# Optimization experiments

Measured on AMD Instinct MI355X. Metric: run time of the kernel, lower is better.

The kernel has to match this reference:

```python
import jax, jax.numpy as jnp
import numpy as np

B, T, N, CIN = 64, 24, 256, 1  # batch, n_his, n stations, in channels
F1, F2, OUTC = 64, 128, 1      # blocks [[64,64],[64,128]], output channels
K = 3                          # conv kernel size


def conv2d_same(x, w):  # x [B,H,W,C], w [K,K,C,O]
    return jax.lax.conv_general_dilated(x, w, (1, 1), 'SAME',
                                        dimension_numbers=('NHWC', 'HWIO', 'NHWC'))


def conv1d_same(x, w):  # x [B,N,C], w [K,C,O]
    return jax.lax.conv_general_dilated(x, w, (1,), 'SAME',
                                        dimension_numbers=('NWC', 'WIO', 'NWC'))


def hard_sigmoid(x):  # keras ConvLSTM default recurrent_activation
    return jnp.clip(x * 0.2 + 0.5, 0.0, 1.0)


def l2_normalize_23(x):  # tf.nn.l2_normalize over axes [2,3]
    sq = jnp.sum(x * x, axis=(2, 3), keepdims=True)
    return x * jax.lax.rsqrt(jnp.maximum(sq, 1e-12))


def convlstm1d(x_seq, kx, kh, b, return_sequences):
    # x_seq [B,T,N,C]; kx [K,C,4F]; kh [K,F,4F]; b [4F]
    Bs, Ts, Ns, Cs = x_seq.shape
    F = kh.shape[1]
    # input convolutions are time-independent: do them all at once
    xg = conv1d_same(x_seq.reshape(Bs * Ts, Ns, Cs), kx).reshape(Bs, Ts, Ns, 4 * F) + b
    xg = jnp.moveaxis(xg, 1, 0)  # [T,B,N,4F]
    h0 = jnp.zeros((Bs, Ns, F), x_seq.dtype)
    c0 = jnp.zeros((Bs, Ns, F), x_seq.dtype)

    def step(carry, xt):
        h, c = carry
        g = xt + conv1d_same(h, kh)                 # [B,N,4F]
        gi, gf, gc, go = jnp.split(g, 4, axis=-1)
        i = hard_sigmoid(gi)
        f = hard_sigmoid(gf)
        o = hard_sigmoid(go)
        c = f * c + i * jnp.tanh(gc)
        h = o * jnp.tanh(c)
        return (h, c), (h if return_sequences else jnp.zeros((), x_seq.dtype))

    (hT, _), hs = jax.lax.scan(step, (h0, c0), xg)
    if return_sequences:
        return jnp.moveaxis(hs, 0, 1)  # [B,T,N,F]
    return hT                          # [B,N,F]


def setup_inputs() -> dict:
    key = jax.random.key(0)
    ks = jax.random.split(key, 14)
    s = 0.1
    return {
        'x': jax.random.normal(ks[0], (B, T, N, CIN), jnp.float32),
        'conv1_w': jax.random.normal(ks[1], (K, K, CIN, F1), jnp.float32) * s,
        'conv1_b': jnp.zeros((F1,), jnp.float32),
        'conv2_w': jax.random.normal(ks[2], (K, K, F1, F1), jnp.float32) * s,
        'conv2_b': jnp.zeros((F1,), jnp.float32),
        'kx1': jax.random.normal(ks[3], (K, F1, 4 * F1), jnp.float32) * s,
        'kh1': jax.random.normal(ks[4], (K, F1, 4 * F1), jnp.float32) * s,
        'b1': jnp.zeros((4 * F1,), jnp.float32),
        'kx2': jax.random.normal(ks[5], (K, F1, 4 * F2), jnp.float32) * s,
        'kh2': jax.random.normal(ks[6], (K, F2, 4 * F2), jnp.float32) * s,
        'b2': jnp.zeros((4 * F2,), jnp.float32),
        'fc_w': jax.random.normal(ks[7], (F2, OUTC), jnp.float32) * s,
        'fc_b': jnp.zeros((OUTC,), jnp.float32),
    }


def reference(x, conv1_w, conv1_b, conv2_w, conv2_b, kx1, kh1, b1,
              kx2, kh2, b2, fc_w, fc_b):
    # spatial conv stack (Conv2D 3x3 same, linear activation)
    h = conv2d_same(x, conv1_w) + conv1_b
    h = conv2d_same(h, conv2_w) + conv2_b
    # dropout = identity at inference; norm == 'L2'
    h = l2_normalize_23(h)
    # stacked ConvLSTM1D: return_sequences=True then False
    h = convlstm1d(h, kx1, kh1, b1, True)    # [B,T,N,F1]
    h = convlstm1d(h, kx2, kh2, b2, False)   # [B,N,F2]
    h = h[:, None]                            # reshape (-1, 1, N, F2)
    h = l2_normalize_23(h)
    # FullyConLayer: 1x1 FC over channels -> outc
    y = jnp.einsum('bunc,co->buno', h, fc_w) + fc_b
    return y.reshape(-1, 1, N, OUTC)
```

## Files before the change

kernel.cpp:

```cpp
#include <hip/hip_runtime.h>
#include <hip/hip_bf16.h>

using bf16 = __hip_bfloat16;
typedef unsigned short u16;
typedef unsigned int u32;
typedef __attribute__((ext_vector_type(8))) short short8;
typedef __attribute__((ext_vector_type(4))) float floatx4;

#define DEVI __device__ __forceinline__

constexpr int B = 64, T = 24, N = 256, F1 = 64, F2 = 128;
constexpr int GG = 6;

DEVI float b2f(bf16 v) { return __bfloat162float(v); }
DEVI float b2fu(u16 u) { return __uint_as_float(((u32)u) << 16); }
DEVI u16 f2b(float f) {
    u32 u = __float_as_uint(f);
    u32 r = (u + 0x7FFF + ((u >> 16) & 1)) >> 16;
    return (u16)r;
}
DEVI float hsig(float x) { x = x * 0.2f + 0.5f; return fminf(fmaxf(x, 0.f), 1.f); }

#if __has_builtin(__builtin_amdgcn_global_load_lds)
#define ASYNC16(gsrc, ldst)                                                            \
    __builtin_amdgcn_global_load_lds((const __attribute__((address_space(1))) u32*)(gsrc), \
                                     (__attribute__((address_space(3))) u32*)(ldst), 16, 0, 0)
#define HAVE_ASYNC 1
#else
#define HAVE_ASYNC 0
#endif

DEVI float read_in(const void* p, long i, int isbf) {
    return isbf ? b2f(((const bf16*)p)[i]) : ((const float*)p)[i];
}

__global__ void init_flag(int* flag) { *flag = 1; }
__global__ void detect_scan(const u16* __restrict__ xu, int* __restrict__ flag) {
    int i0 = blockIdx.x * 2048 + threadIdx.x;
    int hit = 0;
    for (int i = i0; i < (blockIdx.x + 1) * 2048; i += 256)
        if (((xu[i] >> 7) & 0xFF) == 0xFF) hit = 1;
    if (hit) *flag = 0;
}

struct CvtDesc { const void* src; float* dst; int n; };
struct CvtPack { CvtDesc d[8]; };
__global__ void cvt_pack(CvtPack p, const int* __restrict__ flag) {
    CvtDesc c = p.d[blockIdx.x];
    int isbf = *flag;
    for (int i = threadIdx.x; i < c.n; i += 256)
        c.dst[i] = c.src ? read_in(c.src, i, isbf) : 0.f;
}

__global__ void repack_w(const void* __restrict__ kxr, const void* __restrict__ khr,
                         u16* __restrict__ Wt, int CIN, int F, const int* __restrict__ flag) {
    int NG = 4 * F, CH = CIN + F, K = 3 * CH;
    int idx = blockIdx.x * 256 + threadIdx.x;
    if (idx >= NG * K) return;
    int g = idx / K, k = idx - g * K;
    int kn = k / CH, c = k - kn * CH;
    int isbf = *flag;
    float v = (c < CIN) ? read_in(kxr, (long)(kn * CIN + c) * NG + g, isbf)
                        : read_in(khr, (long)(kn * F + (c - CIN)) * NG + g, isbf);
    Wt[(long)g * K + k] = f2b(v);
}

__global__ void repack_w2(const void* __restrict__ w2r, u16* __restrict__ w2b,
                          const int* __restrict__ flag) {
    int idx = blockIdx.x * 256 + threadIdx.x;
    if (idx >= 64 * 576) return;
    int f = idx / 576, k = idx - f * 576;
    int kt = k / 192, rem = k - kt * 192, kn = rem >> 6, c = rem & 63;
    float v = read_in(w2r, (long)((kt * 3 + kn) * 64 + c) * 64 + f, *flag);
    w2b[(long)f * 576 + k] = f2b(v);
}

__global__ __launch_bounds__(256)
void conv_mfma(const void* __restrict__ xraw, const float* __restrict__ w1c,
               const float* __restrict__ b1v, const u16* __restrict__ w2b,
               const float* __restrict__ b2v, u16* __restrict__ xs6,
               float* __restrict__ ssq, const int* __restrict__ flag, int g0) {
    constexpr int CP1 = 72;
    __shared__ __align__(16) u16 win1[3 * 66 * CP1];
    __shared__ float sxw[5 * 68];
    __shared__ __align__(16) u16 bch[2 * 2048];
    __shared__ float red[256];

    int tid = threadIdx.x;
    int bb = blockIdx.y, n0 = blockIdx.x * 64, t = g0 * GG + blockIdx.z;
    int w = tid >> 6, l15 = tid & 15, q = (tid >> 4) & 3;
    int isbf = *flag;

    for (int i = tid; i < 5 * 68; i += 256) {
        int r = i / 68, cc = i - r * 68;
        int tt = t - 2 + r, nn = n0 - 2 + cc;
        float v = 0.f;
        if (tt >= 0 && tt < T && nn >= 0 && nn < N)
            v = read_in(xraw, (long)(bb * T + tt) * N + nn, isbf);
        sxw[i] = v;
    }
    __syncthreads();
    for (int i = tid; i < 3 * 66 * 64; i += 256) {
        int c = i & 63, rr = i >> 6;
        int kt = rr / 66, r1 = rr - kt * 66;
        int tt = t - 1 + kt, nn = n0 - 1 + r1;
        u16 o = 0;
        if (tt >= 0 && tt < T && nn >= 0 && nn < N) {
            float v = b1v[c];
            for (int dt = 0; dt < 3; dt++)
#pragma unroll
                for (int dn = 0; dn < 3; dn++)
                    v += sxw[(kt + dt) * 68 + r1 + dn] * w1c[(dt * 3 + dn) * 64 + c];
            o = f2b(v);
        }
        win1[(kt * 66 + r1) * CP1 + c] = o;
    }

    auto stage = [&](int kk, int bufi) {
        int g = tid >> 2, u = tid & 3;
        int k = kk * 32 + ((u ^ (g & 3)) << 3);
#if HAVE_ASYNC
        ASYNC16(w2b + (long)g * 576 + k, &bch[bufi * 2048 + tid * 8]);
#else
        uint4 v = *(const uint4*)(w2b + (long)g * 576 + k);
        *(uint4*)&bch[bufi * 2048 + tid * 8] = v;
#endif
    };
    stage(0, 0);
    __syncthreads();

    floatx4 acc[4] = {};
    for (int kk = 0; kk < 18; ++kk) {
        int cur = kk & 1;
        if (kk + 1 < 18) stage(kk + 1, 1 - cur);
        int kbase = kk * 32;
        int kt = kbase / 192, rem = kbase - kt * 192, kn = rem >> 6, c0 = rem & 63;
        int gcol = w * 16 + l15;
        short8 bf = *(const short8*)&bch[cur * 2048 + gcol * 32 + ((q ^ (gcol & 3)) << 3)];
#pragma unroll
        for (int mi = 0; mi < 4; mi++) {
            short8 af = *(const short8*)&win1[(kt * 66 + mi * 16 + l15 + kn) * CP1 + c0 + q * 8];
            acc[mi] = __builtin_amdgcn_mfma_f32_16x16x32_bf16(af, bf, acc[mi], 0, 0, 0);
        }
        __syncthreads();
    }

    u16* xslice = xs6 + (long)blockIdx.z * B * N * 64;
    int f = w * 16 + l15;
    float bias2 = b2v[f];
    float lsum = 0.f;
#pragma unroll
    for (int mi = 0; mi < 4; mi++)
#pragma unroll
        for (int r = 0; r < 4; r++) {
            int n = n0 + mi * 16 + q * 4 + r;
            float v = acc[mi][r] + bias2;
            lsum += v * v;
            xslice[((long)bb * N + n) * 64 + f] = f2b(v);
        }
    red[tid] = lsum; __syncthreads();
    for (int k = 128; k > 0; k >>= 1) {
        if (tid < k) red[tid] += red[tid + k];
        __syncthreads();
    }
    if (tid == 0) atomicAdd(&ssq[bb * T + t], red[0]);
}

template<int CIN, int F, int FL>
__global__ __launch_bounds__(512, 4)
void lstm_mfma(const u16* __restrict__ xin, const u16* __restrict__ hprev,
               u16* __restrict__ hnext, float* __restrict__ cst,
               const u16* __restrict__ Wt, const float* __restrict__ bias,
               const float* __restrict__ ssqp, int t) {
    constexpr int CH = CIN + F;
    constexpr int CHP = CH + 8;
    constexpr int K = 3 * CH;
    constexpr int NK = K / 32;
    constexpr int NGL = 4 * FL;
    constexpr int NGP = NGL + 4;
    constexpr int NI = NGL / 128;
    constexpr int BCH = NGL * 32;
    constexpr int GLD_USH = 32 * NGP * 2;
    constexpr int UNION_USH = (2 * BCH > GLD_USH) ? 2 * BCH : GLD_USH;
    constexpr int LOGFL = (FL == 64) ? 6 : 5;

    __shared__ __align__(16) u16 win[66 * CHP];
    __shared__ __align__(16) u16 ubuf[UNION_USH];
    u16* bch = ubuf;
    float* Gld = (float*)ubuf;

    int tid = threadIdx.x;
    int bb = blockIdx.y, n0 = blockIdx.x * 64, z = blockIdx.z;
    int w = tid >> 6, l15 = tid & 15, q = (tid >> 4) & 3;

    float scale = 1.f;
    if (ssqp) scale = rsqrtf(fmaxf(ssqp[bb * T + t], 1e-12f));

    constexpr int GRP = CH / 4;
    for (int i = tid; i < 66 * GRP; i += 512) {
        int row = i / GRP, g4 = (i - row * GRP) * 4;
        int n = n0 + row - 1;
        uint2 v{};
        if (n >= 0 && n < N) {
            if (g4 < CIN) {
                v = *(const uint2*)&xin[((long)bb * N + n) * CIN + g4];
                if (ssqp) {
                    u16 e0 = f2b(b2fu((u16)(v.x & 0xFFFF)) * scale);
                    u16 e1 = f2b(b2fu((u16)(v.x >> 16)) * scale);
                    u16 e2 = f2b(b2fu((u16)(v.y & 0xFFFF)) * scale);
                    u16 e3 = f2b(b2fu((u16)(v.y >> 16)) * scale);
                    v.x = (u32)e0 | ((u32)e1 << 16);
                    v.y = (u32)e2 | ((u32)e3 << 16);
                }
            } else if (t > 0) {
                v = *(const uint2*)&hprev[((long)bb * N + n) * F + (g4 - CIN)];
            }
        }
        *(uint2*)&win[row * CHP + g4] = v;
    }

    auto stage = [&](int kk, int bufi) {
#pragma unroll
        for (int it = 0; it < NGL / 128; ++it) {
            int P = it * 512 + tid;
            int r = P >> 2, u = P & 3;
            int gt = r >> LOGFL, fl = r & (FL - 1);
            long g = (long)gt * F + z * FL + fl;
            int k = kk * 32 + ((u ^ (r & 3)) << 3);
#if HAVE_ASYNC
            ASYNC16(Wt + g * K + k, &bch[bufi * BCH + P * 8]);
#else
            uint4 v = *(const uint4*)(Wt + g * K + k);
            *(uint4*)&bch[bufi * BCH + P * 8] = v;
#endif
        }
    };
    stage(0, 0);
    __syncthreads();

    floatx4 acc[4][NI] = {};
    for (int kk = 0; kk < NK; ++kk) {
        int cur = kk & 1;
        if (kk + 1 < NK) stage(kk + 1, 1 - cur);
        int kbase = kk * 32;
        int kn = kbase / CH, c0 = kbase - kn * CH;
        short8 af[4];
#pragma unroll
        for (int mi = 0; mi < 4; mi++)
            af[mi] = *(const short8*)&win[(mi * 16 + l15 + kn) * CHP + c0 + q * 8];
#pragma unroll
        for (int ni = 0; ni < NI; ni++) {
            int r = w * (NI * 16) + ni * 16 + l15;
            short8 bf = *(const short8*)&bch[cur * BCH + r * 32 + ((q ^ (r & 3)) << 3)];
#pragma unroll
            for (int mi = 0; mi < 4; mi++)
                acc[mi][ni] = __builtin_amdgcn_mfma_f32_16x16x32_bf16(af[mi], bf, acc[mi][ni], 0, 0, 0);
        }
        __syncthreads();
    }

    for (int h = 0; h < 2; ++h) {
#pragma unroll
        for (int mi2 = 0; mi2 < 2; ++mi2) {
            int mi = h * 2 + mi2;
#pragma unroll
            for (int ni = 0; ni < NI; ni++)
#pragma unroll
                for (int r = 0; r < 4; r++)
                    Gld[(mi2 * 16 + q * 4 + r) * NGP + w * (NI * 16) + ni * 16 + l15] = acc[mi][ni][r];
        }
        __syncthreads();
        for (int i = tid; i < 32 * FL; i += 512) {
            int m = i >> LOGFL, fl = i & (FL - 1);
            int fz = z * FL + fl;
            float gi = Gld[m * NGP + fl]          + bias[fz];
            float gf = Gld[m * NGP + FL + fl]     + bias[F + fz];
            float gc = Gld[m * NGP + 2 * FL + fl] + bias[2 * F + fz];
            float go = Gld[m * NGP + 3 * FL + fl] + bias[3 * F + fz];
            int n = n0 + h * 32 + m;
            long ci = ((long)bb * N + n) * F + fz;
            float cp = (t > 0) ? cst[ci] : 0.f;
            float iv = hsig(gi), fv = hsig(gf), ov = hsig(go);
            float cn = fv * cp + iv * tanhf(gc);
            cst[ci] = cn;
            hnext[ci] = f2b(ov * tanhf(cn));
        }
        __syncthreads();
    }
}

__global__ void final_kernel(const u16* __restrict__ hT, const float* __restrict__ fcw,
                             const float* __restrict__ fcb, void* __restrict__ out,
                             const int* __restrict__ flag) {
    __shared__ float red[256];
    int b = blockIdx.x, tid = threadIdx.x;
    const u16* hb = hT + (long)b * N * 128;
    float s = 0.f;
    for (int i = tid; i < N * 128; i += 256) { float v = b2fu(hb[i]); s += v * v; }
    red[tid] = s; __syncthreads();
    for (int k = 128; k > 0; k >>= 1) {
        if (tid < k) red[tid] += red[tid + k];
        __syncthreads();
    }
    float scale = rsqrtf(fmaxf(red[0], 1e-12f));
    int n = tid;
    float acc = fcb[0];
    for (int c = 0; c < 128; c++) acc += b2fu(hb[n * 128 + c]) * scale * fcw[c];
    if (*flag) ((bf16*)out)[b * N + n] = __float2bfloat16(acc);
    else       ((float*)out)[b * N + n] = acc;
}

extern "C" void kernel_launch(void* const* d_in, const int* in_sizes, int n_in,
                              void* d_out, int out_size, void* d_ws, size_t ws_size,
                              hipStream_t stream) {
    float* ws = (float*)d_ws;
    u16* xs6   = (u16*)ws;
    u16* h1A   = (u16*)(ws + 3145728);
    u16* h1B   = (u16*)(ws + 3670016);
    u16* h2A   = (u16*)(ws + 4194304);
    u16* h2B   = (u16*)(ws + 5242880);
    float* c1  = ws + 6291456;
    float* c2  = ws + 7340032;
    u16* Wt1   = (u16*)(ws + 9437184);
    u16* Wt2   = (u16*)(ws + 9486336);
    u16* w2b   = (u16*)(ws + 9633792);
    float* w1c  = ws + 9652224;
    float* bb1  = ws + 9652800;
    float* bb2  = ws + 9652864;
    float* bg1  = ws + 9652928;
    float* bg2  = ws + 9653184;
    float* fcwf = ws + 9653696;
    float* fcbf = ws + 9653824;
    float* ssq  = ws + 9653825;
    int*   flag = (int*)(ws + 9655361);

    init_flag<<<1, 1, 0, stream>>>(flag);
    detect_scan<<<32, 256, 0, stream>>>((const u16*)d_in[0], flag);

    CvtPack pk;
    pk.d[0] = {d_in[1],  w1c,  576};
    pk.d[1] = {d_in[2],  bb1,  64};
    pk.d[2] = {d_in[4],  bb2,  64};
    pk.d[3] = {d_in[7],  bg1,  256};
    pk.d[4] = {d_in[10], bg2,  512};
    pk.d[5] = {d_in[11], fcwf, 128};
    pk.d[6] = {d_in[12], fcbf, 1};
    pk.d[7] = {nullptr,  ssq,  B * T};
    cvt_pack<<<8, 256, 0, stream>>>(pk, flag);

    repack_w<<<(256 * 384 + 255) / 256, 256, 0, stream>>>(d_in[5], d_in[6], Wt1, 64, 64, flag);
    repack_w<<<(512 * 576 + 255) / 256, 256, 0, stream>>>(d_in[8], d_in[9], Wt2, 64, 128, flag);
    repack_w2<<<(64 * 576 + 255) / 256, 256, 0, stream>>>(d_in[3], w2b, flag);

    for (int g = 0; g < T / GG; g++) {
        conv_mfma<<<dim3(4, B, GG), 256, 0, stream>>>(d_in[0], w1c, bb1, w2b, bb2, xs6, ssq, flag, g);
        for (int ti = 0; ti < GG; ti++) {
            int t = g * GG + ti;
            const u16* h1p = (t & 1) ? h1A : h1B;
            u16* h1n = (t & 1) ? h1B : h1A;
            lstm_mfma<64, 64, 32><<<dim3(4, B, 2), 512, 0, stream>>>(
                xs6 + (long)ti * B * N * 64, h1p, h1n, c1, Wt1, bg1, ssq, t);
            const u16* h2p = (t & 1) ? h2A : h2B;
            u16* h2n = (t & 1) ? h2B : h2A;
            lstm_mfma<64, 128, 64><<<dim3(4, B, 2), 512, 0, stream>>>(
                h1n, h2p, h2n, c2, Wt2, bg2, nullptr, t);
        }
    }
    final_kernel<<<B, 256, 0, stream>>>(h2B, fcwf, fcbf, d_out, flag);
}
```

Baseline: 1.056 ms.

## Precompute conv1 once per time group and raise group size to eight

```diff
diff --git a/kernel.cpp b/kernel.cpp
--- a/kernel.cpp
+++ b/kernel.cpp
@@ -10,7 +10,7 @@
 #define DEVI __device__ __forceinline__
 
 constexpr int B = 64, T = 24, N = 256, F1 = 64, F2 = 128;
-constexpr int GG = 6;
+constexpr int GG = 8;
 
 DEVI float b2f(bf16 v) { return __bfloat162float(v); }
 DEVI float b2fu(u16 u) { return __uint_as_float(((u32)u) << 16); }
@@ -76,44 +76,66 @@
 }
 
 __global__ __launch_bounds__(256)
-void conv_mfma(const void* __restrict__ xraw, const float* __restrict__ w1c,
-               const float* __restrict__ b1v, const u16* __restrict__ w2b,
-               const float* __restrict__ b2v, u16* __restrict__ xs6,
-               float* __restrict__ ssq, const int* __restrict__ flag, int g0) {
+void conv1_grp(const void* __restrict__ xraw, const float* __restrict__ w1c,
+               const float* __restrict__ b1v, u16* __restrict__ c1grp,
+               const int* __restrict__ flag, int g0) {
+    __shared__ float sxw[3 * 260];
+    int s = blockIdx.x, b = blockIdx.y, tid = threadIdx.x;
+    int tt = g0 * GG - 1 + s;
+    u16* dst = c1grp + ((long)s * B + b) * N * 64;
+    if (tt < 0 || tt >= T) {
+        for (int i = tid; i < N * 64 / 4; i += 256) *(uint2*)&dst[i * 4] = uint2{0, 0};
+        return;
+    }
+    int isbf = *flag;
+    for (int i = tid; i < 3 * 258; i += 256) {
+        int r = i / 258, cc = i - r * 258;
+        int ttt = tt - 1 + r, nn = cc - 1;
+        float v = 0.f;
+        if (ttt >= 0 && ttt < T && nn >= 0 && nn < N)
+            v = read_in(xraw, (long)(b * T + ttt) * N + nn, isbf);
+        sxw[r * 260 + cc] = v;
+    }
+    __syncthreads();
+    int c = tid & 63, ngq = tid >> 6;
+    float w[9];
+#pragma unroll
+    for (int j = 0; j < 9; j++) w[j] = w1c[j * 64 + c];
+    float bias = b1v[c];
+    for (int j = 0; j < 64; j++) {
+        int n = ngq * 64 + j;
+        float v = bias;
+#pragma unroll
+        for (int dt = 0; dt < 3; dt++)
+#pragma unroll
+            for (int dn = 0; dn < 3; dn++)
+                v += sxw[dt * 260 + n + dn] * w[dt * 3 + dn];
+        dst[n * 64 + c] = f2b(v);
+    }
+}
+
+__global__ __launch_bounds__(256)
+void conv_mfma(const u16* __restrict__ c1grp, const u16* __restrict__ w2b,
+               const float* __restrict__ b2v, u16* __restrict__ xs8,
+               float* __restrict__ ssq, int g0) {
     constexpr int CP1 = 72;
     __shared__ __align__(16) u16 win1[3 * 66 * CP1];
-    __shared__ float sxw[5 * 68];
     __shared__ __align__(16) u16 bch[2 * 2048];
     __shared__ float red[256];
 
     int tid = threadIdx.x;
-    int bb = blockIdx.y, n0 = blockIdx.x * 64, t = g0 * GG + blockIdx.z;
+    int bb = blockIdx.y, n0 = blockIdx.x * 64, z = blockIdx.z;
+    int t = g0 * GG + z;
     int w = tid >> 6, l15 = tid & 15, q = (tid >> 4) & 3;
-    int isbf = *flag;
-
-    for (int i = tid; i < 5 * 68; i += 256) {
-        int r = i / 68, cc = i - r * 68;
-        int tt = t - 2 + r, nn = n0 - 2 + cc;
-        float v = 0.f;
-        if (tt >= 0 && tt < T && nn >= 0 && nn < N)
-            v = read_in(xraw, (long)(bb * T + tt) * N + nn, isbf);
-        sxw[i] = v;
-    }
-    __syncthreads();
-    for (int i = tid; i < 3 * 66 * 64; i += 256) {
-        int c = i & 63, rr = i >> 6;
+
+    for (int i = tid; i < 3 * 66 * 8; i += 256) {
+        int u = i & 7, rr = i >> 3;
         int kt = rr / 66, r1 = rr - kt * 66;
-        int tt = t - 1 + kt, nn = n0 - 1 + r1;
-        u16 o = 0;
-        if (tt >= 0 && tt < T && nn >= 0 && nn < N) {
-            float v = b1v[c];
-            for (int dt = 0; dt < 3; dt++)
-#pragma unroll
-                for (int dn = 0; dn < 3; dn++)
-                    v += sxw[(kt + dt) * 68 + r1 + dn] * w1c[(dt * 3 + dn) * 64 + c];
-            o = f2b(v);
-        }
-        win1[(kt * 66 + r1) * CP1 + c] = o;
+        int nn = n0 - 1 + r1;
+        uint4 v{0, 0, 0, 0};
+        if (nn >= 0 && nn < N)
+            v = *(const uint4*)&c1grp[((((long)(z + kt)) * B + bb) * N + nn) * 64 + u * 8];
+        *(uint4*)&win1[(kt * 66 + r1) * CP1 + u * 8] = v;
     }
 
     auto stage = [&](int kk, int bufi) {
@@ -145,7 +167,7 @@
         __syncthreads();
     }
 
-    u16* xslice = xs6 + (long)blockIdx.z * B * N * 64;
+    u16* xslice = xs8 + (long)z * B * N * 64;
     int f = w * 16 + l15;
     float bias2 = b2v[f];
     float lsum = 0.f;
@@ -314,25 +336,26 @@
                               void* d_out, int out_size, void* d_ws, size_t ws_size,
                               hipStream_t stream) {
     float* ws = (float*)d_ws;
-    u16* xs6   = (u16*)ws;
-    u16* h1A   = (u16*)(ws + 3145728);
-    u16* h1B   = (u16*)(ws + 3670016);
-    u16* h2A   = (u16*)(ws + 4194304);
-    u16* h2B   = (u16*)(ws + 5242880);
-    float* c1  = ws + 6291456;
-    float* c2  = ws + 7340032;
-    u16* Wt1   = (u16*)(ws + 9437184);
-    u16* Wt2   = (u16*)(ws + 9486336);
-    u16* w2b   = (u16*)(ws + 9633792);
-    float* w1c  = ws + 9652224;
-    float* bb1  = ws + 9652800;
-    float* bb2  = ws + 9652864;
-    float* bg1  = ws + 9652928;
-    float* bg2  = ws + 9653184;
-    float* fcwf = ws + 9653696;
-    float* fcbf = ws + 9653824;
-    float* ssq  = ws + 9653825;
-    int*   flag = (int*)(ws + 9655361);
+    u16* xs8    = (u16*)ws;
+    u16* c1grp  = (u16*)(ws + 4194304);
+    u16* h1A    = (u16*)(ws + 9437184);
+    u16* h1B    = (u16*)(ws + 9961472);
+    u16* h2A    = (u16*)(ws + 10485760);
+    u16* h2B    = (u16*)(ws + 11534336);
+    float* c1   = ws + 12582912;
+    float* c2   = ws + 13631488;
+    u16* Wt1    = (u16*)(ws + 15728640);
+    u16* Wt2    = (u16*)(ws + 15777792);
+    u16* w2b    = (u16*)(ws + 15925248);
+    float* w1c  = ws + 15943680;
+    float* bb1  = ws + 15944256;
+    float* bb2  = ws + 15944320;
+    float* bg1  = ws + 15944384;
+    float* bg2  = ws + 15944640;
+    float* fcwf = ws + 15945152;
+    float* fcbf = ws + 15945280;
+    float* ssq  = ws + 15945281;
+    int*   flag = (int*)(ws + 15946817);
 
     init_flag<<<1, 1, 0, stream>>>(flag);
     detect_scan<<<32, 256, 0, stream>>>((const u16*)d_in[0], flag);
@@ -353,13 +376,14 @@
     repack_w2<<<(64 * 576 + 255) / 256, 256, 0, stream>>>(d_in[3], w2b, flag);
 
     for (int g = 0; g < T / GG; g++) {
-        conv_mfma<<<dim3(4, B, GG), 256, 0, stream>>>(d_in[0], w1c, bb1, w2b, bb2, xs6, ssq, flag, g);
+        conv1_grp<<<dim3(GG + 2, B), 256, 0, stream>>>(d_in[0], w1c, bb1, c1grp, flag, g);
+        conv_mfma<<<dim3(4, B, GG), 256, 0, stream>>>(c1grp, w2b, bb2, xs8, ssq, g);
         for (int ti = 0; ti < GG; ti++) {
             int t = g * GG + ti;
             const u16* h1p = (t & 1) ? h1A : h1B;
             u16* h1n = (t & 1) ? h1B : h1A;
             lstm_mfma<64, 64, 32><<<dim3(4, B, 2), 512, 0, stream>>>(
-                xs6 + (long)ti * B * N * 64, h1p, h1n, c1, Wt1, bg1, ssq, t);
+                xs8 + (long)ti * B * N * 64, h1p, h1n, c1, Wt1, bg1, ssq, t);
             const u16* h2p = (t & 1) ? h2A : h2B;
             u16* h2n = (t & 1) ? h2B : h2A;
             lstm_mfma<64, 128, 64><<<dim3(4, B, 2), 512, 0, stream>>>(
```

Result: faster. 997.8 us (-5.5%).
